# Kernel tuning notes

Hardware: AMD Instinct MI355X
Metric: run time of the kernel (lower is better)

Reference implementation:

```python
import jax, jax.numpy as jnp
import numpy as np

N_CUST = 500000
N_FUND = 50000
N_EDGE = 4000000
D_CUST = 101
D_FUND = 1
HID = 64


def setup_inputs() -> dict:
    key = jax.random.key(0)
    ks = jax.random.split(key, 16)
    s = lambda fan_in: 1.0 / np.sqrt(fan_in)
    return {
        "x_customer": jax.random.normal(ks[0], (N_CUST, D_CUST), jnp.float32),
        "x_fund": jax.random.normal(ks[1], (N_FUND, D_FUND), jnp.float32),
        "src_fund": jax.random.randint(ks[2], (N_EDGE,), 0, N_FUND, jnp.int64),
        "dst_customer": jax.random.randint(ks[3], (N_EDGE,), 0, N_CUST, jnp.int64),
        # per-node-type input projections
        "W_cust": jax.random.uniform(ks[4], (D_CUST, HID), jnp.float32, -s(D_CUST), s(D_CUST)),
        "b_cust": jax.random.uniform(ks[5], (HID,), jnp.float32, -s(D_CUST), s(D_CUST)),
        "W_fund": jax.random.uniform(ks[6], (D_FUND, HID), jnp.float32, -s(D_FUND), s(D_FUND)),
        "b_fund": jax.random.uniform(ks[7], (HID,), jnp.float32, -s(D_FUND), s(D_FUND)),
        # SAGEConv fund->customer: lin_l (neighbor aggr, bias) + lin_r (self, no bias)
        "W_l": jax.random.uniform(ks[8], (HID, HID), jnp.float32, -s(HID), s(HID)),
        "b_l": jax.random.uniform(ks[9], (HID,), jnp.float32, -s(HID), s(HID)),
        "W_r": jax.random.uniform(ks[10], (HID, HID), jnp.float32, -s(HID), s(HID)),
        # output head
        "W_out": jax.random.uniform(ks[11], (HID, 2), jnp.float32, -s(HID), s(HID)),
        "b_out": jax.random.uniform(ks[12], (2,), jnp.float32, -s(HID), s(HID)),
    }


def reference(x_customer, x_fund, src_fund, dst_customer,
              W_cust, b_cust, W_fund, b_fund, W_l, b_l, W_r, W_out, b_out):
    # per-node-type linear + relu
    h_c = jax.nn.relu(x_customer @ W_cust + b_cust)  # [N_CUST, HID]
    h_f = jax.nn.relu(x_fund @ W_fund + b_fund)      # [N_FUND, HID]

    # SAGEConv (fund -> customer): gather src fund features per edge,
    # mean-aggregate by destination customer (scatter-sum / count)
    msgs = h_f[src_fund]  # [N_EDGE, HID]
    summed = jax.ops.segment_sum(msgs, dst_customer, num_segments=N_CUST)
    cnt = jax.ops.segment_sum(jnp.ones((msgs.shape[0],), msgs.dtype),
                              dst_customer, num_segments=N_CUST)
    mean = summed / jnp.maximum(cnt, 1.0)[:, None]

    out_c = mean @ W_l + b_l + h_c @ W_r  # SAGE: lin_l(aggr) + lin_r(self)
    return out_c @ W_out + b_out          # [N_CUST, 2]
```

## Files before the change

kernel.cpp:

```cpp
#include <hip/hip_runtime.h>
#include <stdint.h>

#define N_CUST 500000
#define N_FUND 50000
#define N_EDGE 4000000
#define D_CUST 101
#define HID 64

#define NB   512
#define EPB  ((N_EDGE + NB - 1) / NB)
#define CB   512
#define NBKT ((N_CUST + CB - 1) / CB)
#define CAP  5120
#define GPAD 32

typedef float float4u __attribute__((ext_vector_type(4), aligned(4)));
using frag_ab = __attribute__((ext_vector_type(8))) short;
using frag_cd = __attribute__((ext_vector_type(4))) float;

struct __align__(16) Accum { float g0, g1, cnt, pad; };

__device__ __forceinline__ short f2bf(float f) {
    unsigned u = __float_as_uint(f);
    u += 0x7fffu + ((u >> 16) & 1u);
    return (short)(u >> 16);
}

__global__ __launch_bounds__(256) void k_gf(
    const float* __restrict__ x_fund,
    const float* __restrict__ W_fund,
    const float* __restrict__ b_fund,
    const float* __restrict__ W_l,
    const float* __restrict__ W_r,
    const float* __restrict__ W_out,
    const float* __restrict__ Wc,
    const float* __restrict__ b_l,
    const float* __restrict__ b_out,
    float2* __restrict__ gf,
    frag_ab* __restrict__ wcb,
    float* __restrict__ Bt,
    float* __restrict__ c2,
    unsigned* __restrict__ gcur,
    float4* __restrict__ Az)
{
    __shared__ float sAf[128];
    __shared__ float sWf[64];
    __shared__ float sBf[64];
    int t = threadIdx.x;

    if (Az != nullptr) {
        float4 z4 = make_float4(0.f, 0.f, 0.f, 0.f);
        for (int i = blockIdx.x * 256 + t; i < N_CUST; i += gridDim.x * 256)
            Az[i] = z4;
    }

    if (t < 128) {
        int h = t >> 1, j = t & 1;
        float s = 0.f;
        for (int k = 0; k < 64; ++k)
            s = fmaf(W_l[h * 64 + k], W_out[k * 2 + j], s);
        sAf[t] = s;
    } else if (t < 192) {
        sWf[t - 128] = W_fund[t - 128];
    } else {
        sBf[t - 192] = b_fund[t - 192];
    }
    __syncthreads();

    int f = blockIdx.x * 256 + t;
    if (f < N_FUND) {
        float xf = x_fund[f];
        float g0 = 0.f, g1 = 0.f;
        #pragma unroll
        for (int h = 0; h < 64; ++h) {
            float hf = fmaxf(fmaf(xf, sWf[h], sBf[h]), 0.f);
            g0 = fmaf(hf, sAf[2 * h + 0], g0);
            g1 = fmaf(hf, sAf[2 * h + 1], g1);
        }
        gf[f] = make_float2(g0, g1);
    }

    if (blockIdx.x == 0) {
        for (int k = t; k < NBKT * GPAD; k += 256) gcur[k] = 0u;
        if (t < 128) {
            int h = t >> 1, j = t & 1;
            float s = 0.f;
            for (int k = 0; k < 64; ++k)
                s = fmaf(W_r[h * 64 + k], W_out[k * 2 + j], s);
            Bt[t] = s;
        } else if (t < 130) {
            int j = t - 128;
            float s = b_out[j];
            for (int k = 0; k < 64; ++k)
                s = fmaf(b_l[k], W_out[k * 2 + j], s);
            c2[j] = s;
        }
        for (int sidx = t; sidx < 1024; sidx += 256) {
            int fidx = sidx >> 6, l = sidx & 63;
            int c = l & 15, q = l >> 4;
            int nt = fidx >> 2, kc = fidx & 3;
            frag_ab fr;
            #pragma unroll
            for (int j = 0; j < 8; ++j) {
                int kk = kc * 32 + q * 8 + j;
                int h  = nt * 16 + c;
                fr[j] = (kk < D_CUST) ? f2bf(Wc[kk * HID + h]) : (short)0;
            }
            wcb[sidx] = fr;
        }
    }
}

__global__ __launch_bounds__(256) void k_reorder(
    const int* __restrict__ src, const int* __restrict__ dst,
    unsigned* __restrict__ gcur, unsigned* __restrict__ recs)
{
    __shared__ unsigned hist[NBKT];
    __shared__ unsigned localOff[NBKT];
    __shared__ unsigned cur[NBKT];
    __shared__ unsigned baseG[NBKT];
    __shared__ unsigned ldsRec[EPB];

    int t = threadIdx.x, b = blockIdx.x;
    int e0 = b * EPB, e1 = min(e0 + EPB, N_EDGE);

    for (int k = t; k < NBKT; k += 256) hist[k] = 0;
    __syncthreads();
    for (int e = e0 + t; e < e1; e += 256)
        atomicAdd(&hist[((unsigned)dst[e]) >> 9], 1u);
    __syncthreads();

    if (t < 64) {
        unsigned v[16], pre[16], run = 0;
        #pragma unroll
        for (int j = 0; j < 16; ++j) {
            int idx = t * 16 + j;
            v[j] = (idx < NBKT) ? hist[idx] : 0u;
            pre[j] = run; run += v[j];
        }
        unsigned sc = run;
        #pragma unroll
        for (int d = 1; d < 64; d <<= 1) {
            unsigned n = __shfl_up(sc, d, 64);
            if (t >= d) sc += n;
        }
        unsigned lane_excl = sc - run;
        #pragma unroll
        for (int j = 0; j < 16; ++j) {
            int idx = t * 16 + j;
            if (idx < NBKT) {
                localOff[idx] = lane_excl + pre[j];
                cur[idx]      = lane_excl + pre[j];
            }
        }
    }
    __syncthreads();

    for (int k = t; k < NBKT; k += 256) {
        unsigned h = hist[k];
        baseG[k] = h ? ((unsigned)k * CAP + atomicAdd(&gcur[k * GPAD], h)) : 0u;
    }

    for (int e = e0 + t; e < e1; e += 256) {
        unsigned d = (unsigned)dst[e];
        unsigned s = (unsigned)src[e];
        unsigned k = d >> 9;
        unsigned p = atomicAdd(&cur[k], 1u);
        ldsRec[p] = s | ((d & 511u) << 16);
    }
    __syncthreads();

    for (int k = t; k < NBKT; k += 256) {
        unsigned i0 = localOff[k], i1 = cur[k];
        unsigned g = baseG[k];
        unsigned gend = ((unsigned)k + 1u) * CAP;
        for (unsigned i = i0; i < i1 && g < gend; ++i, ++g)
            recs[g] = ldsRec[i];
    }
}

__global__ __launch_bounds__(512) void k_bucket(
    const unsigned* __restrict__ recs, const unsigned* __restrict__ gcur,
    const float2* __restrict__ gf,
    const float* __restrict__ x, const float* __restrict__ bc,
    const frag_ab* __restrict__ wcb, const float* __restrict__ Bt,
    const float* __restrict__ c2,
    float2* __restrict__ out)
{
    __shared__ float s0[CB], s1[CB], scn[CB];
    __shared__ float sBt[128];
    __shared__ float zb[8][16 * 68];

    int t = threadIdx.x, k = blockIdx.x;
    int w = t >> 6, lane = t & 63;
    int c = lane & 15, q = lane >> 4;
    float* z = zb[w];

    if (t < 128) sBt[t] = Bt[t];
    for (int cc = t; cc < CB; cc += 512) { s0[cc] = 0.f; s1[cc] = 0.f; scn[cc] = 0.f; }
    __syncthreads();

    unsigned n = min(gcur[(unsigned)k * GPAD], (unsigned)CAP);
    unsigned r0 = (unsigned)k * CAP;
    for (unsigned i = r0 + t; i < r0 + n; i += 512) {
        unsigned r = recs[i];
        float2 g = gf[r & 0xFFFFu];
        unsigned dl = r >> 16;
        atomicAdd(&s0[dl], g.x);
        atomicAdd(&s1[dl], g.y);
        atomicAdd(&scn[dl], 1.f);
    }

    frag_ab bfrag[16];
    #pragma unroll
    for (int f = 0; f < 16; ++f) bfrag[f] = wcb[f * 64 + lane];
    float bcv[4];
    #pragma unroll
    for (int nt = 0; nt < 4; ++nt) bcv[nt] = bc[nt * 16 + c];
    float c20 = c2[0], c21 = c2[1];
    __syncthreads();

    int cust0 = k * CB;
    int n_tiles = min(CB / 16, (N_CUST - cust0) >> 4);

    for (int tl = w; tl < n_tiles; tl += 8) {
        int lrow = tl * 16 + c;
        int row = cust0 + lrow;
        const float* xr = x + (size_t)row * D_CUST;
        frag_ab af[4];
        #pragma unroll
        for (int kc = 0; kc < 3; ++kc) {
            float4u lo = *(const float4u*)(xr + kc * 32 + q * 8);
            float4u hi = *(const float4u*)(xr + kc * 32 + q * 8 + 4);
            frag_ab f;
            f[0]=f2bf(lo[0]); f[1]=f2bf(lo[1]); f[2]=f2bf(lo[2]); f[3]=f2bf(lo[3]);
            f[4]=f2bf(hi[0]); f[5]=f2bf(hi[1]); f[6]=f2bf(hi[2]); f[7]=f2bf(hi[3]);
            af[kc] = f;
        }
        {
            frag_ab f = {0,0,0,0,0,0,0,0};
            if (q == 0) {
                float4u lo = *(const float4u*)(xr + 96);
                f[0]=f2bf(lo[0]); f[1]=f2bf(lo[1]); f[2]=f2bf(lo[2]); f[3]=f2bf(lo[3]);
                f[4]=f2bf(xr[100]);
            }
            af[3] = f;
        }
        frag_cd acc[4];
        #pragma unroll
        for (int nt = 0; nt < 4; ++nt)
            acc[nt] = (frag_cd){bcv[nt], bcv[nt], bcv[nt], bcv[nt]};
        #pragma unroll
        for (int kc = 0; kc < 4; ++kc)
            #pragma unroll
            for (int nt = 0; nt < 4; ++nt)
                acc[nt] = __builtin_amdgcn_mfma_f32_16x16x32_bf16(
                    af[kc], bfrag[nt * 4 + kc], acc[nt], 0, 0, 0);

        #pragma unroll
        for (int nt = 0; nt < 4; ++nt)
            #pragma unroll
            for (int i = 0; i < 4; ++i)
                z[(q * 4 + i) * 68 + nt * 16 + c] = fmaxf(acc[nt][i], 0.f);

        float p0 = 0.f, p1 = 0.f;
        #pragma unroll
        for (int j4 = 0; j4 < 4; ++j4) {
            float4u zv = *(const float4u*)(z + c * 68 + q * 16 + j4 * 4);
            float4u b0 = *(const float4u*)(sBt + q * 32 + j4 * 8);
            float4u b1 = *(const float4u*)(sBt + q * 32 + j4 * 8 + 4);
            p0 = fmaf(zv[0], b0[0], p0); p1 = fmaf(zv[0], b0[1], p1);
            p0 = fmaf(zv[1], b0[2], p0); p1 = fmaf(zv[1], b0[3], p1);
            p0 = fmaf(zv[2], b1[0], p0); p1 = fmaf(zv[2], b1[1], p1);
            p0 = fmaf(zv[3], b1[2], p0); p1 = fmaf(zv[3], b1[3], p1);
        }
        p0 += __shfl_xor(p0, 16, 64); p0 += __shfl_xor(p0, 32, 64);
        p1 += __shfl_xor(p1, 16, 64); p1 += __shfl_xor(p1, 32, 64);
        if (q == 0) {
            float inv = 1.0f / fmaxf(scn[lrow], 1.0f);
            out[row] = make_float2(fmaf(s0[lrow], inv, p0 + c20),
                                   fmaf(s1[lrow], inv, p1 + c21));
        }
    }
}

__global__ __launch_bounds__(256) void k_scatter_direct(
    const int* __restrict__ src, const int* __restrict__ dst,
    const float2* __restrict__ gf, Accum* __restrict__ A)
{
    int stride = gridDim.x * 256;
    for (int e = blockIdx.x * 256 + threadIdx.x; e < N_EDGE; e += stride) {
        int s = src[e], d = dst[e];
        float2 g = gf[s];
        unsafeAtomicAdd(&A[d].g0, g.x);
        unsafeAtomicAdd(&A[d].g1, g.y);
        unsafeAtomicAdd(&A[d].cnt, 1.0f);
    }
}

__global__ __launch_bounds__(256) void k_mean(
    const Accum* __restrict__ A, float2* __restrict__ mean2)
{
    int i = blockIdx.x * 256 + threadIdx.x;
    if (i < N_CUST) {
        Accum a = A[i];
        float inv = 1.0f / fmaxf(a.cnt, 1.0f);
        mean2[i] = make_float2(a.g0 * inv, a.g1 * inv);
    }
}

__global__ __launch_bounds__(256) void k_gemm(
    const float* __restrict__ x, const float* __restrict__ bc,
    const frag_ab* __restrict__ wcb, const float* __restrict__ Bt,
    const float* __restrict__ c2, const float2* __restrict__ mean2,
    float2* __restrict__ out)
{
    __shared__ float sBt[128];
    __shared__ float zb[4][16 * 68];

    int t = threadIdx.x;
    int w = t >> 6, lane = t & 63;
    int c = lane & 15, q = lane >> 4;
    float* z = zb[w];

    if (t < 128) sBt[t] = Bt[t];
    frag_ab bfrag[16];
    #pragma unroll
    for (int f = 0; f < 16; ++f) bfrag[f] = wcb[f * 64 + lane];
    float bcv[4];
    #pragma unroll
    for (int nt = 0; nt < 4; ++nt) bcv[nt] = bc[nt * 16 + c];
    float c20 = c2[0], c21 = c2[1];
    __syncthreads();

    const int NT = N_CUST / 16;
    for (int tl = blockIdx.x * 4 + w; tl < NT; tl += gridDim.x * 4) {
        int row0 = tl * 16;
        const float* xr = x + (size_t)(row0 + c) * D_CUST;
        frag_ab af[4];
        #pragma unroll
        for (int kc = 0; kc < 3; ++kc) {
            float4u lo = *(const float4u*)(xr + kc * 32 + q * 8);
            float4u hi = *(const float4u*)(xr + kc * 32 + q * 8 + 4);
            frag_ab f;
            f[0]=f2bf(lo[0]); f[1]=f2bf(lo[1]); f[2]=f2bf(lo[2]); f[3]=f2bf(lo[3]);
            f[4]=f2bf(hi[0]); f[5]=f2bf(hi[1]); f[6]=f2bf(hi[2]); f[7]=f2bf(hi[3]);
            af[kc] = f;
        }
        {
            frag_ab f = {0,0,0,0,0,0,0,0};
            if (q == 0) {
                float4u lo = *(const float4u*)(xr + 96);
                f[0]=f2bf(lo[0]); f[1]=f2bf(lo[1]); f[2]=f2bf(lo[2]); f[3]=f2bf(lo[3]);
                f[4]=f2bf(xr[100]);
            }
            af[3] = f;
        }
        frag_cd acc[4];
        #pragma unroll
        for (int nt = 0; nt < 4; ++nt)
            acc[nt] = (frag_cd){bcv[nt], bcv[nt], bcv[nt], bcv[nt]};
        #pragma unroll
        for (int kc = 0; kc < 4; ++kc)
            #pragma unroll
            for (int nt = 0; nt < 4; ++nt)
                acc[nt] = __builtin_amdgcn_mfma_f32_16x16x32_bf16(
                    af[kc], bfrag[nt * 4 + kc], acc[nt], 0, 0, 0);
        #pragma unroll
        for (int nt = 0; nt < 4; ++nt)
            #pragma unroll
            for (int i = 0; i < 4; ++i)
                z[(q * 4 + i) * 68 + nt * 16 + c] = fmaxf(acc[nt][i], 0.f);
        float p0 = 0.f, p1 = 0.f;
        #pragma unroll
        for (int j4 = 0; j4 < 4; ++j4) {
            float4u zv = *(const float4u*)(z + c * 68 + q * 16 + j4 * 4);
            float4u b0 = *(const float4u*)(sBt + q * 32 + j4 * 8);
            float4u b1 = *(const float4u*)(sBt + q * 32 + j4 * 8 + 4);
            p0 = fmaf(zv[0], b0[0], p0); p1 = fmaf(zv[0], b0[1], p1);
            p0 = fmaf(zv[1], b0[2], p0); p1 = fmaf(zv[1], b0[3], p1);
            p0 = fmaf(zv[2], b1[0], p0); p1 = fmaf(zv[2], b1[1], p1);
            p0 = fmaf(zv[3], b1[2], p0); p1 = fmaf(zv[3], b1[3], p1);
        }
        p0 += __shfl_xor(p0, 16, 64); p0 += __shfl_xor(p0, 32, 64);
        p1 += __shfl_xor(p1, 16, 64); p1 += __shfl_xor(p1, 32, 64);
        if (q == 0) {
            float2 m = mean2[row0 + c];
            out[row0 + c] = make_float2(p0 + c20 + m.x, p1 + c21 + m.y);
        }
    }
}

extern "C" void kernel_launch(void* const* d_in, const int* in_sizes, int n_in,
                              void* d_out, int out_size, void* d_ws, size_t ws_size,
                              hipStream_t stream) {
    const float* x_customer = (const float*)d_in[0];
    const float* x_fund     = (const float*)d_in[1];
    const int*   src_fund   = (const int*)d_in[2];
    const int*   dst_cust   = (const int*)d_in[3];
    const float* W_cust     = (const float*)d_in[4];
    const float* b_cust     = (const float*)d_in[5];
    const float* W_fund     = (const float*)d_in[6];
    const float* b_fund     = (const float*)d_in[7];
    const float* W_l        = (const float*)d_in[8];
    const float* b_l        = (const float*)d_in[9];
    const float* W_r        = (const float*)d_in[10];
    const float* W_out      = (const float*)d_in[11];
    const float* b_out      = (const float*)d_in[12];

    char* ws = (char*)d_ws;
    const size_t NEED_FAST = 20550976ull;

    if (ws_size >= NEED_FAST) {
        unsigned* recs = (unsigned*)(ws);
        float2*   gf   = (float2*)  (ws + 20008960);
        frag_ab*  wcb  = (frag_ab*) (ws + 20408960);
        float*    Bt   = (float*)   (ws + 20425344);
        float*    c2   = (float*)   (ws + 20425856);
        unsigned* gcur = (unsigned*)(ws + 20425920);

        k_gf<<<256, 256, 0, stream>>>(
            x_fund, W_fund, b_fund, W_l, W_r, W_out, W_cust, b_l, b_out,
            gf, wcb, Bt, c2, gcur, nullptr);
        k_reorder<<<NB, 256, 0, stream>>>(src_fund, dst_cust, gcur, recs);
        k_bucket<<<NBKT, 512, 0, stream>>>(
            recs, gcur, gf, x_customer, b_cust, wcb, Bt, c2, (float2*)d_out);
    } else {
        Accum*    A    = (Accum*)   (ws);
        float2*   mn2  = (float2*)  (ws + 8000000);
        float2*   gf   = (float2*)  (ws + 12000000);
        frag_ab*  wcb  = (frag_ab*) (ws + 12400000);
        float*    Bt   = (float*)   (ws + 12416384);
        float*    c2   = (float*)   (ws + 12416896);
        unsigned* gcur = (unsigned*)(ws + 12416960);

        k_gf<<<256, 256, 0, stream>>>(
            x_fund, W_fund, b_fund, W_l, W_r, W_out, W_cust, b_l, b_out,
            gf, wcb, Bt, c2, gcur, (float4*)A);
        k_scatter_direct<<<2048, 256, 0, stream>>>(src_fund, dst_cust, gf, A);
        k_mean<<<(N_CUST + 255) / 256, 256, 0, stream>>>(A, mn2);
        k_gemm<<<2048, 256, 0, stream>>>(
            x_customer, b_cust, wcb, Bt, c2, mn2, (float2*)d_out);
    }
}
```

Before: 459.7 us.

## Warp-specialize bucket kernel and parallelize per-bucket record writeout in reorder

```diff
diff --git a/kernel.cpp b/kernel.cpp
--- a/kernel.cpp
+++ b/kernel.cpp
@@ -120,9 +120,11 @@
     __shared__ unsigned cur[NBKT];
     __shared__ unsigned baseG[NBKT];
     __shared__ unsigned ldsRec[EPB];
+    __shared__ unsigned short ldsBkt[EPB];
 
     int t = threadIdx.x, b = blockIdx.x;
     int e0 = b * EPB, e1 = min(e0 + EPB, N_EDGE);
+    int cntE = e1 - e0;
 
     for (int k = t; k < NBKT; k += 256) hist[k] = 0;
     __syncthreads();
@@ -167,19 +169,18 @@
         unsigned k = d >> 9;
         unsigned p = atomicAdd(&cur[k], 1u);
         ldsRec[p] = s | ((d & 511u) << 16);
-    }
-    __syncthreads();
-
-    for (int k = t; k < NBKT; k += 256) {
-        unsigned i0 = localOff[k], i1 = cur[k];
-        unsigned g = baseG[k];
-        unsigned gend = ((unsigned)k + 1u) * CAP;
-        for (unsigned i = i0; i < i1 && g < gend; ++i, ++g)
-            recs[g] = ldsRec[i];
-    }
-}
-
-__global__ __launch_bounds__(512) void k_bucket(
+        ldsBkt[p] = (unsigned short)k;
+    }
+    __syncthreads();
+
+    for (int i = t; i < cntE; i += 256) {
+        unsigned k = ldsBkt[i];
+        unsigned g = baseG[k] + (i - localOff[k]);
+        if (g < (k + 1u) * CAP) recs[g] = ldsRec[i];
+    }
+}
+
+__global__ __launch_bounds__(256) void k_bucket(
     const unsigned* __restrict__ recs, const unsigned* __restrict__ gcur,
     const float2* __restrict__ gf,
     const float* __restrict__ x, const float* __restrict__ bc,
@@ -189,98 +190,120 @@
 {
     __shared__ float s0[CB], s1[CB], scn[CB];
     __shared__ float sBt[128];
-    __shared__ float zb[8][16 * 68];
+    __shared__ float pbuf[2 * CB];
+    __shared__ float zb[3][16 * 68];
 
     int t = threadIdx.x, k = blockIdx.x;
     int w = t >> 6, lane = t & 63;
     int c = lane & 15, q = lane >> 4;
-    float* z = zb[w];
 
     if (t < 128) sBt[t] = Bt[t];
-    for (int cc = t; cc < CB; cc += 512) { s0[cc] = 0.f; s1[cc] = 0.f; scn[cc] = 0.f; }
-    __syncthreads();
-
-    unsigned n = min(gcur[(unsigned)k * GPAD], (unsigned)CAP);
-    unsigned r0 = (unsigned)k * CAP;
-    for (unsigned i = r0 + t; i < r0 + n; i += 512) {
-        unsigned r = recs[i];
-        float2 g = gf[r & 0xFFFFu];
-        unsigned dl = r >> 16;
-        atomicAdd(&s0[dl], g.x);
-        atomicAdd(&s1[dl], g.y);
-        atomicAdd(&scn[dl], 1.f);
-    }
-
-    frag_ab bfrag[16];
-    #pragma unroll
-    for (int f = 0; f < 16; ++f) bfrag[f] = wcb[f * 64 + lane];
-    float bcv[4];
-    #pragma unroll
-    for (int nt = 0; nt < 4; ++nt) bcv[nt] = bc[nt * 16 + c];
-    float c20 = c2[0], c21 = c2[1];
+    for (int cc = t; cc < CB; cc += 256) { s0[cc] = 0.f; s1[cc] = 0.f; scn[cc] = 0.f; }
     __syncthreads();
 
     int cust0 = k * CB;
-    int n_tiles = min(CB / 16, (N_CUST - cust0) >> 4);
-
-    for (int tl = w; tl < n_tiles; tl += 8) {
-        int lrow = tl * 16 + c;
-        int row = cust0 + lrow;
-        const float* xr = x + (size_t)row * D_CUST;
-        frag_ab af[4];
-        #pragma unroll
-        for (int kc = 0; kc < 3; ++kc) {
-            float4u lo = *(const float4u*)(xr + kc * 32 + q * 8);
-            float4u hi = *(const float4u*)(xr + kc * 32 + q * 8 + 4);
-            frag_ab f;
-            f[0]=f2bf(lo[0]); f[1]=f2bf(lo[1]); f[2]=f2bf(lo[2]); f[3]=f2bf(lo[3]);
-            f[4]=f2bf(hi[0]); f[5]=f2bf(hi[1]); f[6]=f2bf(hi[2]); f[7]=f2bf(hi[3]);
-            af[kc] = f;
-        }
-        {
-            frag_ab f = {0,0,0,0,0,0,0,0};
+    int ncust = min(CB, N_CUST - cust0);
+    int n_tiles = ncust >> 4;
+
+    if (w == 3) {
+        unsigned n = min(gcur[(unsigned)k * GPAD], (unsigned)CAP);
+        const unsigned* rp = recs + (size_t)k * CAP;
+        unsigned i = (unsigned)lane * 4u;
+        for (; i + 4u <= n; i += 256u) {
+            uint4 rr = *(const uint4*)(rp + i);
+            float2 ga = gf[rr.x & 0xFFFFu];
+            float2 gb = gf[rr.y & 0xFFFFu];
+            float2 gc = gf[rr.z & 0xFFFFu];
+            float2 gd = gf[rr.w & 0xFFFFu];
+            unsigned da = rr.x >> 16, db = rr.y >> 16;
+            unsigned dc = rr.z >> 16, dd = rr.w >> 16;
+            atomicAdd(&s0[da], ga.x); atomicAdd(&s1[da], ga.y); atomicAdd(&scn[da], 1.f);
+            atomicAdd(&s0[db], gb.x); atomicAdd(&s1[db], gb.y); atomicAdd(&scn[db], 1.f);
+            atomicAdd(&s0[dc], gc.x); atomicAdd(&s1[dc], gc.y); atomicAdd(&scn[dc], 1.f);
+            atomicAdd(&s0[dd], gd.x); atomicAdd(&s1[dd], gd.y); atomicAdd(&scn[dd], 1.f);
+        }
+        unsigned base = n & ~3u;
+        if ((unsigned)lane < (n & 3u)) {
+            unsigned r = rp[base + lane];
+            float2 g = gf[r & 0xFFFFu];
+            unsigned dl = r >> 16;
+            atomicAdd(&s0[dl], g.x); atomicAdd(&s1[dl], g.y); atomicAdd(&scn[dl], 1.f);
+        }
+    } else {
+        float* z = zb[w];
+        frag_ab bfrag[16];
+        #pragma unroll
+        for (int f = 0; f < 16; ++f) bfrag[f] = wcb[f * 64 + lane];
+        float bcv[4];
+        #pragma unroll
+        for (int nt = 0; nt < 4; ++nt) bcv[nt] = bc[nt * 16 + c];
+        float c20 = c2[0], c21 = c2[1];
+
+        for (int tl = w; tl < n_tiles; tl += 3) {
+            int lrow = tl * 16 + c;
+            int row = cust0 + lrow;
+            const float* xr = x + (size_t)row * D_CUST;
+            frag_ab af[4];
+            #pragma unroll
+            for (int kc = 0; kc < 3; ++kc) {
+                float4u lo = *(const float4u*)(xr + kc * 32 + q * 8);
+                float4u hi = *(const float4u*)(xr + kc * 32 + q * 8 + 4);
+                frag_ab f;
+                f[0]=f2bf(lo[0]); f[1]=f2bf(lo[1]); f[2]=f2bf(lo[2]); f[3]=f2bf(lo[3]);
+                f[4]=f2bf(hi[0]); f[5]=f2bf(hi[1]); f[6]=f2bf(hi[2]); f[7]=f2bf(hi[3]);
+                af[kc] = f;
+            }
+            {
+                frag_ab f = {0,0,0,0,0,0,0,0};
+                if (q == 0) {
+                    float4u lo = *(const float4u*)(xr + 96);
+                    f[0]=f2bf(lo[0]); f[1]=f2bf(lo[1]); f[2]=f2bf(lo[2]); f[3]=f2bf(lo[3]);
+                    f[4]=f2bf(xr[100]);
+                }
+                af[3] = f;
+            }
+            frag_cd acc[4];
+            #pragma unroll
+            for (int nt = 0; nt < 4; ++nt)
+                acc[nt] = (frag_cd){bcv[nt], bcv[nt], bcv[nt], bcv[nt]};
+            #pragma unroll
+            for (int kc = 0; kc < 4; ++kc)
+                #pragma unroll
+                for (int nt = 0; nt < 4; ++nt)
+                    acc[nt] = __builtin_amdgcn_mfma_f32_16x16x32_bf16(
+                        af[kc], bfrag[nt * 4 + kc], acc[nt], 0, 0, 0);
+
+            #pragma unroll
+            for (int nt = 0; nt < 4; ++nt)
+                #pragma unroll
+                for (int i = 0; i < 4; ++i)
+                    z[(q * 4 + i) * 68 + nt * 16 + c] = fmaxf(acc[nt][i], 0.f);
+
+            float p0 = 0.f, p1 = 0.f;
+            #pragma unroll
+            for (int j4 = 0; j4 < 4; ++j4) {
+                float4u zv = *(const float4u*)(z + c * 68 + q * 16 + j4 * 4);
+                float4u b0 = *(const float4u*)(sBt + q * 32 + j4 * 8);
+                float4u b1 = *(const float4u*)(sBt + q * 32 + j4 * 8 + 4);
+                p0 = fmaf(zv[0], b0[0], p0); p1 = fmaf(zv[0], b0[1], p1);
+                p0 = fmaf(zv[1], b0[2], p0); p1 = fmaf(zv[1], b0[3], p1);
+                p0 = fmaf(zv[2], b1[0], p0); p1 = fmaf(zv[2], b1[1], p1);
+                p0 = fmaf(zv[3], b1[2], p0); p1 = fmaf(zv[3], b1[3], p1);
+            }
+            p0 += __shfl_xor(p0, 16, 64); p0 += __shfl_xor(p0, 32, 64);
+            p1 += __shfl_xor(p1, 16, 64); p1 += __shfl_xor(p1, 32, 64);
             if (q == 0) {
-                float4u lo = *(const float4u*)(xr + 96);
-                f[0]=f2bf(lo[0]); f[1]=f2bf(lo[1]); f[2]=f2bf(lo[2]); f[3]=f2bf(lo[3]);
-                f[4]=f2bf(xr[100]);
-            }
-            af[3] = f;
-        }
-        frag_cd acc[4];
-        #pragma unroll
-        for (int nt = 0; nt < 4; ++nt)
-            acc[nt] = (frag_cd){bcv[nt], bcv[nt], bcv[nt], bcv[nt]};
-        #pragma unroll
-        for (int kc = 0; kc < 4; ++kc)
-            #pragma unroll
-            for (int nt = 0; nt < 4; ++nt)
-                acc[nt] = __builtin_amdgcn_mfma_f32_16x16x32_bf16(
-                    af[kc], bfrag[nt * 4 + kc], acc[nt], 0, 0, 0);
-
-        #pragma unroll
-        for (int nt = 0; nt < 4; ++nt)
-            #pragma unroll
-            for (int i = 0; i < 4; ++i)
-                z[(q * 4 + i) * 68 + nt * 16 + c] = fmaxf(acc[nt][i], 0.f);
-
-        float p0 = 0.f, p1 = 0.f;
-        #pragma unroll
-        for (int j4 = 0; j4 < 4; ++j4) {
-            float4u zv = *(const float4u*)(z + c * 68 + q * 16 + j4 * 4);
-            float4u b0 = *(const float4u*)(sBt + q * 32 + j4 * 8);
-            float4u b1 = *(const float4u*)(sBt + q * 32 + j4 * 8 + 4);
-            p0 = fmaf(zv[0], b0[0], p0); p1 = fmaf(zv[0], b0[1], p1);
-            p0 = fmaf(zv[1], b0[2], p0); p1 = fmaf(zv[1], b0[3], p1);
-            p0 = fmaf(zv[2], b1[0], p0); p1 = fmaf(zv[2], b1[1], p1);
-            p0 = fmaf(zv[3], b1[2], p0); p1 = fmaf(zv[3], b1[3], p1);
-        }
-        p0 += __shfl_xor(p0, 16, 64); p0 += __shfl_xor(p0, 32, 64);
-        p1 += __shfl_xor(p1, 16, 64); p1 += __shfl_xor(p1, 32, 64);
-        if (q == 0) {
-            float inv = 1.0f / fmaxf(scn[lrow], 1.0f);
-            out[row] = make_float2(fmaf(s0[lrow], inv, p0 + c20),
-                                   fmaf(s1[lrow], inv, p1 + c21));
-        }
+                pbuf[2 * lrow]     = p0 + c20;
+                pbuf[2 * lrow + 1] = p1 + c21;
+            }
+        }
+    }
+    __syncthreads();
+
+    for (int cc = t; cc < ncust; cc += 256) {
+        float inv = 1.0f / fmaxf(scn[cc], 1.0f);
+        out[cust0 + cc] = make_float2(fmaf(s0[cc], inv, pbuf[2 * cc]),
+                                      fmaf(s1[cc], inv, pbuf[2 * cc + 1]));
     }
 }
 
@@ -423,7 +446,7 @@
             x_fund, W_fund, b_fund, W_l, W_r, W_out, W_cust, b_l, b_out,
             gf, wcb, Bt, c2, gcur, nullptr);
         k_reorder<<<NB, 256, 0, stream>>>(src_fund, dst_cust, gcur, recs);
-        k_bucket<<<NBKT, 512, 0, stream>>>(
+        k_bucket<<<NBKT, 256, 0, stream>>>(
             recs, gcur, gf, x_customer, b_cust, wcb, Bt, c2, (float2*)d_out);
     } else {
         Accum*    A    = (Accum*)   (ws);
```

After: 420.3 us. 8.6% less time.
